# Performance work log

Hardware: AMD Instinct MI355X
Metric: run time of the kernel (lower is better)

Reference implementation:

```python
import jax, jax.numpy as jnp
import numpy as np
from jax.scipy.special import logsumexp

N, T, K, V = 32, 4096, 128, 50000

def setup_inputs() -> dict:
    key = jax.random.key(0)
    ks = jax.random.split(key, 6)
    return {
        "x": jax.random.randint(ks[0], (N, T), 0, V, dtype=jnp.int64),
        "start_w": jax.random.normal(ks[1], (K, 1), dtype=jnp.float32),
        "start_b": jax.random.normal(ks[2], (K,), dtype=jnp.float32),
        "cluster_trans_w": jax.random.uniform(ks[3], (K * K, 1), dtype=jnp.float32, minval=-1.0, maxval=1.0),
        "emb_cluster_w": jax.random.normal(ks[4], (K, K), dtype=jnp.float32),
        "cluster_vocab_w": jax.random.uniform(ks[5], (V, K), dtype=jnp.float32, minval=-1.0, maxval=1.0),
    }

def reference(x, start_w, start_b, cluster_trans_w, emb_cluster_w, cluster_vocab_w):
    # dummy = ones(N,1) => Linear(1,.) collapses to weight[:,0] (+ bias), identical per batch row
    tran = jax.nn.log_softmax(cluster_trans_w[:, 0].reshape(K, K), axis=-1)      # (K,K) log p(k'|k)
    alpha0 = jnp.broadcast_to(start_w[:, 0] + start_b, (N, K))                    # (N,K)
    # Emissions[k,v] = log_softmax_v(emb_cluster.weight[k] @ cluster_vocab.weight.T)
    emis_t = jax.nn.log_softmax(emb_cluster_w @ cluster_vocab_w.T, axis=-1).T     # (V,K)

    def step(alpha, w_t):
        a = logsumexp(alpha[:, :, None] + tran[None, :, :], axis=1)               # (N,K)
        a = a + emis_t[w_t]                                                        # gather emission log-probs
        return a, None

    alpha_T, _ = jax.lax.scan(step, alpha0, x.T)                                  # scan over T timesteps
    return -jnp.mean(logsumexp(alpha_T, axis=1))
```

## Files before the change

kernel.cpp:

```cpp
#include <hip/hip_runtime.h>

typedef unsigned int uint;
typedef unsigned short ushort;
typedef uint4 uint4_a __attribute__((may_alias));
typedef uint ui4v __attribute__((ext_vector_type(4)));
typedef float fx4 __attribute__((ext_vector_type(4)));
typedef short s8v __attribute__((ext_vector_type(8)));

__device__ __forceinline__ uint bfpack(float a, float b) {
  uint ua = __float_as_uint(a), ub = __float_as_uint(b);
  ua += 0x7fffu + ((ua >> 16) & 1u);
  ub += 0x7fffu + ((ub >> 16) & 1u);
  return (ua >> 16) | (ub & 0xffff0000u);
}
__device__ __forceinline__ float bflo(uint d) { return __uint_as_float(d << 16); }
__device__ __forceinline__ float bfhi(uint d) { return __uint_as_float(d & 0xffff0000u); }
__device__ __forceinline__ ushort bfr(float s) {
  return (ushort)((__float_as_uint(s) + 0x8000u) >> 16);
}

#if __has_builtin(__builtin_amdgcn_fdot2_f32_bf16)
#define HAVE_BFDOT 1
typedef __bf16 v2bf __attribute__((ext_vector_type(2)));
__device__ __forceinline__ float dot2bf(uint a, uint b, float c) {
  return __builtin_amdgcn_fdot2_f32_bf16(__builtin_bit_cast(v2bf, a),
                                         __builtin_bit_cast(v2bf, b), c, false);
}
#else
#define HAVE_BFDOT 0
#endif

__global__ __launch_bounds__(128) void k_tran(const float* __restrict__ w,
                                              uint* __restrict__ Tcol) {
  __shared__ float rowLSE[128];
  int tid = threadIdx.x;
  const float4* w4 = (const float4*)(w + tid * 128);
  float se = 0.f;
  #pragma unroll 8
  for (int i = 0; i < 32; ++i) {
    float4 v = w4[i];
    se += __expf(v.x) + __expf(v.y) + __expf(v.z) + __expf(v.w);
  }
  rowLSE[tid] = __logf(se);
  __syncthreads();
  int j = tid & 63;
  int c = 2 * blockIdx.x + (tid >> 6);
  float a = __expf(w[(2 * j) * 128 + c]     - rowLSE[2 * j]);
  float b = __expf(w[(2 * j + 1) * 128 + c] - rowLSE[2 * j + 1]);
  Tcol[c * 64 + j] = bfpack(a, b);
}

__global__ __launch_bounds__(256) void k_logits(const float* __restrict__ emb,
    const float* __restrict__ vocab, uint* __restrict__ qtbl,
    float* __restrict__ S_glob, int V) {
  __shared__ float S_part[128];
  int tid = threadIdx.x;
  int kt = tid & 15, vt = tid >> 4;
  int k0 = kt * 8;
  int vbase = blockIdx.x * 64 + vt * 4;
  if (tid < 128) S_part[tid] = 0.f;
  __syncthreads();

  float acc[4][8];
  #pragma unroll
  for (int i = 0; i < 4; ++i)
    #pragma unroll
    for (int r = 0; r < 8; ++r) acc[i][r] = 0.f;

  int vidx[4];
  #pragma unroll
  for (int i = 0; i < 4; ++i) { int vv = vbase + i; vidx[i] = (vv < V) ? vv : (V - 1); }

  const float4* emb4 = (const float4*)emb;
  const float4* voc4 = (const float4*)vocab;
  for (int jb = 0; jb < 32; ++jb) {
    float4 e4[8];
    #pragma unroll
    for (int r = 0; r < 8; ++r) e4[r] = emb4[(k0 + r) * 32 + jb];
    #pragma unroll
    for (int i = 0; i < 4; ++i) {
      float4 va = voc4[(size_t)vidx[i] * 32 + jb];
      #pragma unroll
      for (int r = 0; r < 8; ++r)
        acc[i][r] += va.x * e4[r].x + va.y * e4[r].y + va.z * e4[r].z + va.w * e4[r].w;
    }
  }

  float sume[8];
  #pragma unroll
  for (int r = 0; r < 8; ++r) sume[r] = 0.f;
  #pragma unroll
  for (int i = 0; i < 4; ++i) {
    int vv = vbase + i;
    if (vv < V) {
      #pragma unroll
      for (int r = 0; r < 8; ++r) sume[r] += __expf(acc[i][r]);
      uint4 st;
      st.x = bfpack(acc[i][0], acc[i][1]);
      st.y = bfpack(acc[i][2], acc[i][3]);
      st.z = bfpack(acc[i][4], acc[i][5]);
      st.w = bfpack(acc[i][6], acc[i][7]);
      *((uint4*)(qtbl + (size_t)vv * 64) + kt) = st;
    }
  }
  #pragma unroll
  for (int r = 0; r < 8; ++r) atomicAdd(&S_part[k0 + r], sume[r]);
  __syncthreads();
  if (tid < 128) atomicAdd(&S_glob[tid], S_part[tid]);
}

__global__ __launch_bounds__(256) void k_qtab(uint* __restrict__ qtbl,
    const float* __restrict__ S_glob, float* __restrict__ Emax, int V) {
  int tid = threadIdx.x;
  int l = tid & 63;
  int v = blockIdx.x * 4 + (tid >> 6);
  if (v >= V) return;
  float2 S2 = ((const float2*)S_glob)[l];
  float z0 = __logf(S2.x), z1 = __logf(S2.y);
  size_t off = (size_t)v * 64 + l;
  uint d = qtbl[off];
  float e0 = bflo(d) - z0, e1 = bfhi(d) - z1;
  float m = fmaxf(e0, e1);
  #pragma unroll
  for (int s = 1; s < 64; s <<= 1) m = fmaxf(m, __shfl_xor(m, s, 64));
  float q0 = __expf(e0 - m), q1 = __expf(e1 - m);
  qtbl[off] = bfpack(q0, q1);
  if (l == 0) Emax[v] = m;
}

#define REPB(M) M(0,0) M(0,1) M(0,2) M(0,3) M(1,0) M(1,1) M(1,2) M(1,3) \
                M(2,0) M(2,1) M(2,2) M(2,3) M(3,0) M(3,1) M(3,2) M(3,3) \
                M(4,0) M(4,1) M(4,2) M(4,3) M(5,0) M(5,1) M(5,2) M(5,3) \
                M(6,0) M(6,1) M(6,2) M(6,3) M(7,0) M(7,1) M(7,2) M(7,3)

#define MFMA(a, b, c) __builtin_amdgcn_mfma_f32_16x16x32_bf16( \
    __builtin_bit_cast(s8v, a), __builtin_bit_cast(s8v, b), c, 0, 0, 0)

#define MST0(OUT, BN) \
  OUT##0 = MFMA(tb0_0, BN, zz4); OUT##1 = MFMA(tb1_0, BN, zz4); \
  OUT##2 = MFMA(tb2_0, BN, zz4); OUT##3 = MFMA(tb3_0, BN, zz4); \
  OUT##4 = MFMA(tb4_0, BN, zz4); OUT##5 = MFMA(tb5_0, BN, zz4); \
  OUT##6 = MFMA(tb6_0, BN, zz4); OUT##7 = MFMA(tb7_0, BN, zz4);
#define MSTA(OUT, BN, ks) \
  OUT##0 = MFMA(tb0_##ks, BN, OUT##0); OUT##1 = MFMA(tb1_##ks, BN, OUT##1); \
  OUT##2 = MFMA(tb2_##ks, BN, OUT##2); OUT##3 = MFMA(tb3_##ks, BN, OUT##3); \
  OUT##4 = MFMA(tb4_##ks, BN, OUT##4); OUT##5 = MFMA(tb5_##ks, BN, OUT##5); \
  OUT##6 = MFMA(tb6_##ks, BN, OUT##6); OUT##7 = MFMA(tb7_##ks, BN, OUT##7);

#define PKPAIR(CCA, CCB, QA, QB, DOUT) { \
  float f0 = bflo(QA.x) * rs, f1 = bfhi(QA.x) * rs; \
  float f2 = bflo(QA.y) * rs, f3 = bfhi(QA.y) * rs; \
  float s0 = CCA.x * f0, s1 = CCA.y * f1, s2 = CCA.z * f2, s3 = CCA.w * f3; \
  fm = fmaxf(fm, fmaxf(fmaxf(s0, s1), fmaxf(s2, s3))); \
  uint p0, p1, p2, p3; \
  asm("v_cvt_pk_bf16_f32 %0, %1, %2" : "=v"(p0) : "v"(s0), "v"(s1)); \
  asm("v_cvt_pk_bf16_f32 %0, %1, %2" : "=v"(p1) : "v"(s2), "v"(s3)); \
  float g0 = bflo(QB.x) * rs, g1 = bfhi(QB.x) * rs; \
  float g2 = bflo(QB.y) * rs, g3 = bfhi(QB.y) * rs; \
  float t0 = CCB.x * g0, t1 = CCB.y * g1, t2 = CCB.z * g2, t3 = CCB.w * g3; \
  fm = fmaxf(fm, fmaxf(fmaxf(t0, t1), fmaxf(t2, t3))); \
  asm("v_cvt_pk_bf16_f32 %0, %1, %2" : "=v"(p2) : "v"(t0), "v"(t1)); \
  asm("v_cvt_pk_bf16_f32 %0, %1, %2" : "=v"(p3) : "v"(t2), "v"(t3)); \
  DOUT.x = p0; DOUT.y = p1; DOUT.z = p2; DOUT.w = p3; }

#define PKPAIR_NR(CCA, CCB, QA, QB, DOUT) { \
  float s0 = CCA.x * bflo(QA.x), s1 = CCA.y * bfhi(QA.x); \
  float s2 = CCA.z * bflo(QA.y), s3 = CCA.w * bfhi(QA.y); \
  uint p0, p1, p2, p3; \
  asm("v_cvt_pk_bf16_f32 %0, %1, %2" : "=v"(p0) : "v"(s0), "v"(s1)); \
  asm("v_cvt_pk_bf16_f32 %0, %1, %2" : "=v"(p1) : "v"(s2), "v"(s3)); \
  float t0 = CCB.x * bflo(QB.x), t1 = CCB.y * bfhi(QB.x); \
  float t2 = CCB.z * bflo(QB.y), t3 = CCB.w * bfhi(QB.y); \
  asm("v_cvt_pk_bf16_f32 %0, %1, %2" : "=v"(p2) : "v"(t0), "v"(t1)); \
  asm("v_cvt_pk_bf16_f32 %0, %1, %2" : "=v"(p3) : "v"(t2), "v"(t3)); \
  DOUT.x = p0; DOUT.y = p1; DOUT.z = p2; DOUT.w = p3; }

#define QLD(dst, tk, i) dst = *(const uint2*)(qtbl + ((size_t)(tk) << 6) + 8 * (i) + 2 * quad);

#define QRELOAD(Q, TKREG, FBASE) \
  QLD(Q##0, TKREG, 0) QLD(Q##1, TKREG, 1) QLD(Q##2, TKREG, 2) QLD(Q##3, TKREG, 3) \
  QLD(Q##4, TKREG, 4) QLD(Q##5, TKREG, 5) QLD(Q##6, TKREG, 6) QLD(Q##7, TKREG, 7) \
  { int fi_ = (FBASE) + 4; if (fi_ > 511) fi_ = 511; TKREG = xseg[fi_]; }

#define SLOT_RS(CIN, COUT, Q, TKREG, FBASE) { \
  rs = 1.0f / fmA;  llacc += __log2f(fmA); \
  float fm = 0.f; \
  PKPAIR(CIN##0, CIN##1, Q##0, Q##1, Bs0) \
  MST0(COUT, Bs0) \
  PKPAIR(CIN##2, CIN##3, Q##2, Q##3, Bs1) \
  MSTA(COUT, Bs1, 1) \
  PKPAIR(CIN##4, CIN##5, Q##4, Q##5, Bs2) \
  MSTA(COUT, Bs2, 2) \
  PKPAIR(CIN##6, CIN##7, Q##6, Q##7, Bs3) \
  MSTA(COUT, Bs3, 3) \
  QRELOAD(Q, TKREG, FBASE) \
  fm = fmaxf(fm, __shfl_xor(fm, 16, 64)); \
  fm = fmaxf(fm, __shfl_xor(fm, 32, 64)); \
  fmA = fmaxf(fm, 1e-33f); \
}

#define SLOT_NR(CIN, COUT, Q, TKREG, FBASE) { \
  PKPAIR_NR(CIN##0, CIN##1, Q##0, Q##1, Bs0) \
  MST0(COUT, Bs0) \
  PKPAIR_NR(CIN##2, CIN##3, Q##2, Q##3, Bs1) \
  MSTA(COUT, Bs1, 1) \
  PKPAIR_NR(CIN##4, CIN##5, Q##4, Q##5, Bs2) \
  MSTA(COUT, Bs2, 2) \
  PKPAIR_NR(CIN##6, CIN##7, Q##6, Q##7, Bs3) \
  MSTA(COUT, Bs3, 3) \
  QRELOAD(Q, TKREG, FBASE) \
}

__global__ __attribute__((amdgpu_flat_work_group_size(512, 512), amdgpu_waves_per_eu(2)))
void k_seg(const int* __restrict__ x, const uint* __restrict__ Tcol,
           const uint* __restrict__ qtbl, uint* __restrict__ Pst,
           float* __restrict__ LLseg) {
  int tid = threadIdx.x;
  int wv = tid >> 6, l = tid & 63, c = l & 15, quad = l >> 4;
  int blk = blockIdx.x;
  const int* xseg = x + (size_t)(blk >> 3) * 4096 + (size_t)(blk & 7) * 512;

  #define DECLB(nt, ks) ui4v tb##nt##_##ks;
  REPB(DECLB)
  {
    #define LOADB(nt, ks) { \
      const uint2* t2_ = (const uint2*)(Tcol + (size_t)(16 * (nt) + c) * 64 + 16 * (ks) + 2 * quad); \
      uint2 lo_ = t2_[0], hi_ = t2_[4]; \
      tb##nt##_##ks.x = lo_.x; tb##nt##_##ks.y = lo_.y; \
      tb##nt##_##ks.z = hi_.x; tb##nt##_##ks.w = hi_.y; }
    REPB(LOADB)
    #define PINB(nt, ks) asm volatile("" : "+a"(tb##nt##_##ks));
    REPB(PINB)
  }

  ui4v Bs0, Bs1, Bs2, Bs3;
  {
    uint iv = (quad == (c >> 2)) ? (0x3F80u << (16 * (c & 1))) : 0u;
    int dsel = ((c >> 1) & 1) + 2 * (wv & 1);
    int kssel = wv >> 1;
    Bs0.x = (kssel == 0 && dsel == 0) ? iv : 0u;
    Bs0.y = (kssel == 0 && dsel == 1) ? iv : 0u;
    Bs0.z = (kssel == 0 && dsel == 2) ? iv : 0u;
    Bs0.w = (kssel == 0 && dsel == 3) ? iv : 0u;
    Bs1.x = (kssel == 1 && dsel == 0) ? iv : 0u;
    Bs1.y = (kssel == 1 && dsel == 1) ? iv : 0u;
    Bs1.z = (kssel == 1 && dsel == 2) ? iv : 0u;
    Bs1.w = (kssel == 1 && dsel == 3) ? iv : 0u;
    Bs2.x = (kssel == 2 && dsel == 0) ? iv : 0u;
    Bs2.y = (kssel == 2 && dsel == 1) ? iv : 0u;
    Bs2.z = (kssel == 2 && dsel == 2) ? iv : 0u;
    Bs2.w = (kssel == 2 && dsel == 3) ? iv : 0u;
    Bs3.x = (kssel == 3 && dsel == 0) ? iv : 0u;
    Bs3.y = (kssel == 3 && dsel == 1) ? iv : 0u;
    Bs3.z = (kssel == 3 && dsel == 2) ? iv : 0u;
    Bs3.w = (kssel == 3 && dsel == 3) ? iv : 0u;
  }

  float rs = 1.0f, llacc = 0.0f, fmA = 1.0f;
  fx4 zz4; zz4.x = 0.f; zz4.y = 0.f; zz4.z = 0.f; zz4.w = 0.f;

  fx4 cA0, cA1, cA2, cA3, cA4, cA5, cA6, cA7;
  fx4 cB0, cB1, cB2, cB3, cB4, cB5, cB6, cB7;

  int tk0 = xseg[0], tk1 = xseg[1];
  int tkA = xseg[2], tkB = xseg[3];
  uint2 qc0, qc1, qc2, qc3, qc4, qc5, qc6, qc7;
  uint2 qn0, qn1, qn2, qn3, qn4, qn5, qn6, qn7;
  QLD(qc0, tk0, 0) QLD(qc1, tk0, 1) QLD(qc2, tk0, 2) QLD(qc3, tk0, 3)
  QLD(qc4, tk0, 4) QLD(qc5, tk0, 5) QLD(qc6, tk0, 6) QLD(qc7, tk0, 7)
  QLD(qn0, tk1, 0) QLD(qn1, tk1, 1) QLD(qn2, tk1, 2) QLD(qn3, tk1, 3)
  QLD(qn4, tk1, 4) QLD(qn5, tk1, 5) QLD(qn6, tk1, 6) QLD(qn7, tk1, 7)

  MST0(cA, Bs0) MSTA(cA, Bs1, 1) MSTA(cA, Bs2, 2) MSTA(cA, Bs3, 3)

  if (wv & 1) __builtin_amdgcn_s_sleep(8);

  for (int f4 = 0; f4 < 128; ++f4) {
    int f = f4 * 4;
    SLOT_RS(cA, cB, qc, tkA, f)
    SLOT_NR(cB, cA, qn, tkB, f + 1)
    SLOT_NR(cA, cB, qc, tkA, f + 2)
    SLOT_NR(cB, cA, qn, tkB, f + 3)
  }

  size_t pb = (size_t)blk * 8192 + (size_t)(16 * wv + c) * 64;
  uint2 st;
  st.x = Bs0.x; st.y = Bs0.y; *(uint2*)(Pst + pb +  0 + 2 * quad) = st;
  st.x = Bs0.z; st.y = Bs0.w; *(uint2*)(Pst + pb +  8 + 2 * quad) = st;
  st.x = Bs1.x; st.y = Bs1.y; *(uint2*)(Pst + pb + 16 + 2 * quad) = st;
  st.x = Bs1.z; st.y = Bs1.w; *(uint2*)(Pst + pb + 24 + 2 * quad) = st;
  st.x = Bs2.x; st.y = Bs2.y; *(uint2*)(Pst + pb + 32 + 2 * quad) = st;
  st.x = Bs2.z; st.y = Bs2.w; *(uint2*)(Pst + pb + 40 + 2 * quad) = st;
  st.x = Bs3.x; st.y = Bs3.y; *(uint2*)(Pst + pb + 48 + 2 * quad) = st;
  st.x = Bs3.z; st.y = Bs3.w; *(uint2*)(Pst + pb + 56 + 2 * quad) = st;
  if (quad == 0)
    LLseg[(size_t)blk * 128 + 16 * wv + c] = llacc * 0.6931471805599453f;
}

__global__ __launch_bounds__(256, 1) void k_comb(
    const float* __restrict__ start_w, const float* __restrict__ start_b,
    const uint* __restrict__ Pst, const float* __restrict__ LLseg,
    float* __restrict__ chainLL) {
  __shared__ uint al[64] __attribute__((aligned(16)));
  __shared__ float2 part[4][64];
  int n = blockIdx.x, tid = threadIdx.x;
  int wv = tid >> 6, l = tid & 63;
  float p0 = 0.f, p1 = 0.f, LLacc = 0.f;
  if (wv == 0) {
    float a0i = start_w[2 * l] + start_b[2 * l];
    float a1i = start_w[2 * l + 1] + start_b[2 * l + 1];
    float m = fmaxf(a0i, a1i);
    #pragma unroll
    for (int s = 1; s < 64; s <<= 1) m = fmaxf(m, __shfl_xor(m, s, 64));
    p0 = __expf(a0i - m); p1 = __expf(a1i - m);
    float tot = p0 + p1;
    #pragma unroll
    for (int s = 1; s < 64; s <<= 1) tot += __shfl_xor(tot, s, 64);
    LLacc = m + __logf(tot);
    float inv = 1.0f / tot;
    p0 *= inv; p1 *= inv;
  }
  const uint4_a* u4 = (const uint4_a*)al;

  for (int s = 0; s < 8; ++s) {
    float g = 0.f;
    if (wv == 0) {
      float La = LLseg[(size_t)(n * 8 + s) * 128 + 2 * l];
      float Lb = LLseg[(size_t)(n * 8 + s) * 128 + 2 * l + 1];
      g = fmaxf(La, Lb);
      #pragma unroll
      for (int sh = 1; sh < 64; sh <<= 1) g = fmaxf(g, __shfl_xor(g, sh, 64));
      al[l] = bfpack(p0 * __expf(La - g), p1 * __expf(Lb - g));
    }
    __syncthreads();

    const uint* pb = Pst + (size_t)(n * 8 + s) * 8192;
    float o0 = 0.f, o1 = 0.f;
    #pragma unroll
    for (int ii = 0; ii < 4; ++ii) {
      int i = 4 * wv + ii;
      uint4 uu = u4[i];
      #pragma unroll
      for (int d = 0; d < 4; ++d) {
        uint ad = (d == 0) ? uu.x : (d == 1) ? uu.y : (d == 2) ? uu.z : uu.w;
        uint P0 = pb[(8 * i + 2 * d) * 64 + l];
        uint P1 = pb[(8 * i + 2 * d + 1) * 64 + l];
        float alo = bflo(ad), ahi = bfhi(ad);
        o0 = fmaf(alo, bflo(P0), o0); o0 = fmaf(ahi, bflo(P1), o0);
        o1 = fmaf(alo, bfhi(P0), o1); o1 = fmaf(ahi, bfhi(P1), o1);
      }
    }
    part[wv][l] = make_float2(o0, o1);
    __syncthreads();

    if (wv == 0) {
      float2 x0 = part[0][l], x1 = part[1][l], x2 = part[2][l], x3 = part[3][l];
      float s0 = (x0.x + x1.x) + (x2.x + x3.x);
      float s1 = (x0.y + x1.y) + (x2.y + x3.y);
      float tt = s0 + s1;
      #pragma unroll
      for (int sh = 1; sh < 64; sh <<= 1) tt += __shfl_xor(tt, sh, 64);
      LLacc += g + __logf(tt);
      float it = 1.0f / tt;
      p0 = s0 * it; p1 = s1 * it;
    }
  }
  if (tid == 0) chainLL[n] = LLacc;
}

#define RLU(i) ((uint)__builtin_amdgcn_readlane((int)ud, rbase + (i)))
#if HAVE_BFDOT
#define DOTS \
  uint u0=RLU(0),u1=RLU(1),u2=RLU(2),u3=RLU(3),u4=RLU(4),u5=RLU(5),u6=RLU(6),u7=RLU(7), \
       u8=RLU(8),u9=RLU(9),u10=RLU(10),u11=RLU(11),u12=RLU(12),u13=RLU(13),u14=RLU(14),u15=RLU(15); \
  float A0 = dot2bf(u0, tA0.x, 0.f), A1 = dot2bf(u1, tA0.y, 0.f); \
  float A2 = dot2bf(u2, tA0.z, 0.f), A3 = dot2bf(u3, tA0.w, 0.f); \
  float B0 = dot2bf(u0, tB0.x, 0.f), B1 = dot2bf(u1, tB0.y, 0.f); \
  float B2 = dot2bf(u2, tB0.z, 0.f), B3 = dot2bf(u3, tB0.w, 0.f); \
  A0 = dot2bf(u4, tA1.x, A0); A1 = dot2bf(u5, tA1.y, A1); \
  A2 = dot2bf(u6, tA1.z, A2); A3 = dot2bf(u7, tA1.w, A3); \
  B0 = dot2bf(u4, tB1.x, B0); B1 = dot2bf(u5, tB1.y, B1); \
  B2 = dot2bf(u6, tB1.z, B2); B3 = dot2bf(u7, tB1.w, B3); \
  A0 = dot2bf(u8, tA2.x, A0); A1 = dot2bf(u9, tA2.y, A1); \
  A2 = dot2bf(u10, tA2.z, A2); A3 = dot2bf(u11, tA2.w, A3); \
  B0 = dot2bf(u8, tB2.x, B0); B1 = dot2bf(u9, tB2.y, B1); \
  B2 = dot2bf(u10, tB2.z, B2); B3 = dot2bf(u11, tB2.w, B3); \
  A0 = dot2bf(u12, tA3.x, A0); A1 = dot2bf(u13, tA3.y, A1); \
  A2 = dot2bf(u14, tA3.z, A2); A3 = dot2bf(u15, tA3.w, A3); \
  B0 = dot2bf(u12, tB3.x, B0); B1 = dot2bf(u13, tB3.y, B1); \
  B2 = dot2bf(u14, tB3.z, B2); B3 = dot2bf(u15, tB3.w, B3); \
  float Asum = (A0 + A1) + (A2 + A3), Bsum = (B0 + B1) + (B2 + B3);
#else
#define ACC2(i, AA, BB) { uint tu = RLU(i); float lo = bflo(tu), hi = bfhi(tu); \
  AA += lo * fa##i.x; AA += hi * fa##i.y; BB += lo * fb##i.x; BB += hi * fb##i.y; }
#define DOTS \
  float A0 = 0.f, A1 = 0.f, A2 = 0.f, A3 = 0.f; \
  float B0 = 0.f, B1 = 0.f, B2 = 0.f, B3 = 0.f; \
  ACC2(0, A0, B0) ACC2(1, A1, B1) ACC2(2, A2, B2) ACC2(3, A3, B3) \
  ACC2(4, A0, B0) ACC2(5, A1, B1) ACC2(6, A2, B2) ACC2(7, A3, B3) \
  ACC2(8, A0, B0) ACC2(9, A1, B1) ACC2(10, A2, B2) ACC2(11, A3, B3) \
  ACC2(12, A0, B0) ACC2(13, A1, B1) ACC2(14, A2, B2) ACC2(15, A3, B3) \
  float Asum = (A0 + A1) + (A2 + A3), Bsum = (B0 + B1) + (B2 + B3);
#endif

#define STEPF(j, p) { \
  DOTS \
  *(float2*)&partLDS[(p) * 640 + l * 10 + 2 * wv] = make_float2(Asum, Bsum); \
  asm volatile("s_waitcnt lgkmcnt(0)\ns_barrier" ::: "memory"); \
  const float2* pr = (const float2*)&partLDS[(p) * 640 + l * 10]; \
  float2 x0 = pr[0], x1 = pr[1], x2 = pr[2], x3 = pr[3]; \
  float s0 = (x0.x + x1.x) + (x2.x + x3.x); \
  float s1 = (x0.y + x1.y) + (x2.y + x3.y); \
  float nu0 = s0 * bflo(qc##j), nu1 = s1 * bfhi(qc##j); \
  qc##j = qtbl[(size_t)tk##j * 64 + l]; \
  tk##j = xrow[(tbase + (j) + 16) & 4095]; \
  if ((j) == 7) { \
    float tt = nu0 + nu1; \
    for (int s = 1; s < 64; s <<= 1) tt += __shfl_xor(tt, s, 64); \
    LLacc += __logf(tt); \
    float it = 1.0f / tt; nu0 *= it; nu1 *= it; \
  } \
  ud = bfpack(nu0, nu1); }

__global__ __launch_bounds__(256, 1) void k_chain(const int* __restrict__ x,
    const float* __restrict__ start_w, const float* __restrict__ start_b,
    const uint* __restrict__ Tcol, const uint* __restrict__ qtbl,
    float* __restrict__ chainLL) {
  __shared__ float partLDS[1280];
  int n = blockIdx.x;
  int l = threadIdx.x & 63;
  int wv = __builtin_amdgcn_readfirstlane((int)(threadIdx.x >> 6));
  int rbase = wv * 16;
  const int* xrow = x + (size_t)n * 4096;

  const uint4* ca = (const uint4*)(Tcol + (2 * l) * 64 + rbase);
  const uint4* cb = (const uint4*)(Tcol + (2 * l + 1) * 64 + rbase);
  uint4 tA0 = ca[0], tA1 = ca[1], tA2 = ca[2], tA3 = ca[3];
  uint4 tB0 = cb[0], tB1 = cb[1], tB2 = cb[2], tB3 = cb[3];
#if !HAVE_BFDOT
  float2 fa0 = make_float2(bflo(tA0.x), bfhi(tA0.x)), fa1 = make_float2(bflo(tA0.y), bfhi(tA0.y));
  float2 fa2 = make_float2(bflo(tA0.z), bfhi(tA0.z)), fa3 = make_float2(bflo(tA0.w), bfhi(tA0.w));
  float2 fa4 = make_float2(bflo(tA1.x), bfhi(tA1.x)), fa5 = make_float2(bflo(tA1.y), bfhi(tA1.y));
  float2 fa6 = make_float2(bflo(tA1.z), bfhi(tA1.z)), fa7 = make_float2(bflo(tA1.w), bfhi(tA1.w));
  float2 fa8 = make_float2(bflo(tA2.x), bfhi(tA2.x)), fa9 = make_float2(bflo(tA2.y), bfhi(tA2.y));
  float2 fa10 = make_float2(bflo(tA2.z), bfhi(tA2.z)), fa11 = make_float2(bflo(tA2.w), bfhi(tA2.w));
  float2 fa12 = make_float2(bflo(tA3.x), bfhi(tA3.x)), fa13 = make_float2(bflo(tA3.y), bfhi(tA3.y));
  float2 fa14 = make_float2(bflo(tA3.z), bfhi(tA3.z)), fa15 = make_float2(bflo(tA3.w), bfhi(tA3.w));
  float2 fb0 = make_float2(bflo(tB0.x), bfhi(tB0.x)), fb1 = make_float2(bflo(tB0.y), bfhi(tB0.y));
  float2 fb2 = make_float2(bflo(tB0.z), bfhi(tB0.z)), fb3 = make_float2(bflo(tB0.w), bfhi(tB0.w));
  float2 fb4 = make_float2(bflo(tB1.x), bfhi(tB1.x)), fb5 = make_float2(bflo(tB1.y), bfhi(tB1.y));
  float2 fb6 = make_float2(bflo(tB1.z), bfhi(tB1.z)), fb7 = make_float2(bflo(tB1.w), bfhi(tB1.w));
  float2 fb8 = make_float2(bflo(tB2.x), bfhi(tB2.x)), fb9 = make_float2(bflo(tB2.y), bfhi(tB2.y));
  float2 fb10 = make_float2(bflo(tB2.z), bfhi(tB2.z)), fb11 = make_float2(bflo(tB2.w), bfhi(tB2.w));
  float2 fb12 = make_float2(bflo(tB3.x), bfhi(tB3.x)), fb13 = make_float2(bflo(tB3.y), bfhi(tB3.y));
  float2 fb14 = make_float2(bflo(tB3.z), bfhi(tB3.z)), fb15 = make_float2(bflo(tB3.w), bfhi(tB3.w));
#endif

  float a0i = start_w[2 * l] + start_b[2 * l];
  float a1i = start_w[2 * l + 1] + start_b[2 * l + 1];
  float m = fmaxf(a0i, a1i);
  #pragma unroll
  for (int s = 1; s < 64; s <<= 1) m = fmaxf(m, __shfl_xor(m, s, 64));
  float p0 = __expf(a0i - m), p1 = __expf(a1i - m);
  float tot = p0 + p1;
  #pragma unroll
  for (int s = 1; s < 64; s <<= 1) tot += __shfl_xor(tot, s, 64);
  float LLacc = m + __logf(tot);
  float inv = 1.0f / tot;
  uint ud = bfpack(p0 * inv, p1 * inv);

  uint qc0 = qtbl[(size_t)xrow[0] * 64 + l], qc1 = qtbl[(size_t)xrow[1] * 64 + l];
  uint qc2 = qtbl[(size_t)xrow[2] * 64 + l], qc3 = qtbl[(size_t)xrow[3] * 64 + l];
  uint qc4 = qtbl[(size_t)xrow[4] * 64 + l], qc5 = qtbl[(size_t)xrow[5] * 64 + l];
  uint qc6 = qtbl[(size_t)xrow[6] * 64 + l], qc7 = qtbl[(size_t)xrow[7] * 64 + l];
  int tk0 = xrow[8],  tk1 = xrow[9],  tk2 = xrow[10], tk3 = xrow[11];
  int tk4 = xrow[12], tk5 = xrow[13], tk6 = xrow[14], tk7 = xrow[15];

  for (int t8 = 0; t8 < 512; ++t8) {
    int tbase = t8 * 8;
    STEPF(0, 0) STEPF(1, 1) STEPF(2, 0) STEPF(3, 1)
    STEPF(4, 0) STEPF(5, 1) STEPF(6, 0) STEPF(7, 1)
  }
  if (l == 0 && wv == 0) chainLL[n] = LLacc;
}

__global__ __launch_bounds__(256) void k_emaxsum(const int* __restrict__ x,
    const float* __restrict__ Emax, float* __restrict__ sumE, int NT) {
  int idx = blockIdx.x * 256 + threadIdx.x;
  float s = 0.f;
  for (; idx < NT; idx += 128 * 256) s += Emax[x[idx]];
  #pragma unroll
  for (int mk = 1; mk < 64; mk <<= 1) s += __shfl_xor(s, mk, 64);
  if ((threadIdx.x & 63) == 0) atomicAdd(sumE, s);
}

__global__ void k_final(const float* __restrict__ chainLL, const float* __restrict__ sumE,
                        float* __restrict__ out, int N) {
  int l = threadIdx.x;
  float v = (l < N) ? chainLL[l] : 0.f;
  #pragma unroll
  for (int mk = 1; mk < 64; mk <<= 1) v += __shfl_xor(v, mk, 64);
  if (l == 0) out[0] = -(v + sumE[0]) / (float)N;
}

extern "C" void kernel_launch(void* const* d_in, const int* in_sizes, int n_in,
                              void* d_out, int out_size, void* d_ws, size_t ws_size,
                              hipStream_t stream) {
  if (n_in < 6) return;
  const int*   x       = (const int*)d_in[0];
  const float* start_w = (const float*)d_in[1];
  const float* start_b = (const float*)d_in[2];
  const float* trans_w = (const float*)d_in[3];
  const float* emb_w   = (const float*)d_in[4];
  const float* vocab_w = (const float*)d_in[5];
  int NT = in_sizes[0];
  int N  = NT / 4096;
  int V  = in_sizes[5] / 128;

  char* ws = (char*)d_ws;
  float* S_glob  = (float*)(ws + 0);
  float* sumE    = (float*)(ws + 512);
  float* chainLL = (float*)(ws + 768);
  uint*  Tcol    = (uint*)(ws + 1024);
  float* Emax    = (float*)(ws + 36864);
  uint*  qtbl    = (uint*)(ws + 262144);
  size_t pst_off = 262144 + (size_t)V * 256;
  uint*  Pst     = (uint*)(ws + pst_off);
  size_t llseg_off = pst_off + (size_t)N * 8 * 8192 * 4;
  float* LLseg   = (float*)(ws + llseg_off);
  size_t need    = llseg_off + (size_t)N * 8 * 128 * 4 + 64;

  hipMemsetAsync(d_ws, 0, 1024, stream);
  k_tran<<<dim3(64), dim3(128), 0, stream>>>(trans_w, Tcol);
  k_logits<<<dim3((V + 63) / 64), dim3(256), 0, stream>>>(emb_w, vocab_w, qtbl, S_glob, V);
  k_qtab<<<dim3((V + 3) / 4), dim3(256), 0, stream>>>(qtbl, S_glob, Emax, V);
  if (ws_size >= need) {
    k_seg<<<dim3(N * 8), dim3(512), 0, stream>>>(x, Tcol, qtbl, Pst, LLseg);
    k_comb<<<dim3(N), dim3(256), 0, stream>>>(start_w, start_b, Pst, LLseg, chainLL);
  } else {
    k_chain<<<dim3(N), dim3(256), 0, stream>>>(x, start_w, start_b, Tcol, qtbl, chainLL);
  }
  k_emaxsum<<<dim3(128), dim3(256), 0, stream>>>(x, Emax, sumE, NT);
  k_final<<<dim3(1), dim3(64), 0, stream>>>(chainLL, sumE, (float*)d_out, N);
}
```

Measured before the change: 698.2 us.

## Compute emission logits with bf16 MFMA instead of scalar FP32 FMAs

Replaces the scalar FP32 emission-logit GEMM (50000x128x128) with bf16 MFMA 16x16x32 instructions. A new small kernel pre-packs the embedding matrix into bf16 pairs, and each wave holds it in AGPRs. Vocab rows are converted to bf16 on the fly with v_cvt_pk_bf16_f32. Logits now carry bf16 input rounding, adding precision error, and an extra kernel launch is added. The workspace layout is also reshuffled to make room for the packed embedding.

```diff
diff --git a/kernel.cpp b/kernel.cpp
--- a/kernel.cpp
+++ b/kernel.cpp
@@ -18,6 +18,9 @@
 __device__ __forceinline__ ushort bfr(float s) {
   return (ushort)((__float_as_uint(s) + 0x8000u) >> 16);
 }
+__device__ __forceinline__ uint cvtpk(float a, float b) {
+  uint r; asm("v_cvt_pk_bf16_f32 %0, %1, %2" : "=v"(r) : "v"(a), "v"(b)); return r;
+}
 
 #if __has_builtin(__builtin_amdgcn_fdot2_f32_bf16)
 #define HAVE_BFDOT 1
@@ -29,6 +32,14 @@
 #else
 #define HAVE_BFDOT 0
 #endif
+
+#define REPB(M) M(0,0) M(0,1) M(0,2) M(0,3) M(1,0) M(1,1) M(1,2) M(1,3) \
+                M(2,0) M(2,1) M(2,2) M(2,3) M(3,0) M(3,1) M(3,2) M(3,3) \
+                M(4,0) M(4,1) M(4,2) M(4,3) M(5,0) M(5,1) M(5,2) M(5,3) \
+                M(6,0) M(6,1) M(6,2) M(6,3) M(7,0) M(7,1) M(7,2) M(7,3)
+
+#define MFMA(a, b, c) __builtin_amdgcn_mfma_f32_16x16x32_bf16( \
+    __builtin_bit_cast(s8v, a), __builtin_bit_cast(s8v, b), c, 0, 0, 0)
 
 __global__ __launch_bounds__(128) void k_tran(const float* __restrict__ w,
                                               uint* __restrict__ Tcol) {
@@ -50,61 +61,79 @@
   Tcol[c * 64 + j] = bfpack(a, b);
 }
 
-__global__ __launch_bounds__(256) void k_logits(const float* __restrict__ emb,
-    const float* __restrict__ vocab, uint* __restrict__ qtbl,
-    float* __restrict__ S_glob, int V) {
+__global__ __launch_bounds__(256) void k_epack(const float* __restrict__ emb,
+                                               uint* __restrict__ Ecol) {
+  int t = blockIdx.x * 256 + threadIdx.x;
+  if (t >= 8192) return;
+  float2 e = *(const float2*)(emb + 2 * t);
+  Ecol[t] = bfpack(e.x, e.y);
+}
+
+__global__ __attribute__((amdgpu_flat_work_group_size(256, 256)))
+void k_logits(const float* __restrict__ vocab, const uint* __restrict__ Ecol,
+              uint* __restrict__ qtbl, float* __restrict__ S_glob, int V) {
   __shared__ float S_part[128];
-  int tid = threadIdx.x;
-  int kt = tid & 15, vt = tid >> 4;
-  int k0 = kt * 8;
-  int vbase = blockIdx.x * 64 + vt * 4;
+  int tid = threadIdx.x, wv = tid >> 6, l = tid & 63, c = l & 15, quad = l >> 4;
   if (tid < 128) S_part[tid] = 0.f;
   __syncthreads();
 
-  float acc[4][8];
-  #pragma unroll
-  for (int i = 0; i < 4; ++i)
-    #pragma unroll
-    for (int r = 0; r < 8; ++r) acc[i][r] = 0.f;
-
-  int vidx[4];
-  #pragma unroll
-  for (int i = 0; i < 4; ++i) { int vv = vbase + i; vidx[i] = (vv < V) ? vv : (V - 1); }
-
-  const float4* emb4 = (const float4*)emb;
-  const float4* voc4 = (const float4*)vocab;
-  for (int jb = 0; jb < 32; ++jb) {
-    float4 e4[8];
-    #pragma unroll
-    for (int r = 0; r < 8; ++r) e4[r] = emb4[(k0 + r) * 32 + jb];
-    #pragma unroll
-    for (int i = 0; i < 4; ++i) {
-      float4 va = voc4[(size_t)vidx[i] * 32 + jb];
-      #pragma unroll
-      for (int r = 0; r < 8; ++r)
-        acc[i][r] += va.x * e4[r].x + va.y * e4[r].y + va.z * e4[r].z + va.w * e4[r].w;
-    }
-  }
-
-  float sume[8];
-  #pragma unroll
-  for (int r = 0; r < 8; ++r) sume[r] = 0.f;
-  #pragma unroll
-  for (int i = 0; i < 4; ++i) {
-    int vv = vbase + i;
-    if (vv < V) {
-      #pragma unroll
-      for (int r = 0; r < 8; ++r) sume[r] += __expf(acc[i][r]);
-      uint4 st;
-      st.x = bfpack(acc[i][0], acc[i][1]);
-      st.y = bfpack(acc[i][2], acc[i][3]);
-      st.z = bfpack(acc[i][4], acc[i][5]);
-      st.w = bfpack(acc[i][6], acc[i][7]);
-      *((uint4*)(qtbl + (size_t)vv * 64) + kt) = st;
-    }
-  }
-  #pragma unroll
-  for (int r = 0; r < 8; ++r) atomicAdd(&S_part[k0 + r], sume[r]);
+  int vb = blockIdx.x * 64 + wv * 16;
+  int vrow = vb + c; if (vrow > V - 1) vrow = V - 1;
+
+  #define DECLE(kt, ks) ui4v eb##kt##_##ks;
+  REPB(DECLE)
+  {
+    #define LOADE(kt, ks) { \
+      const uint2* t2_ = (const uint2*)(Ecol + (size_t)(16 * (kt) + c) * 64 + 16 * (ks) + 2 * quad); \
+      uint2 lo_ = t2_[0], hi_ = t2_[4]; \
+      eb##kt##_##ks.x = lo_.x; eb##kt##_##ks.y = lo_.y; \
+      eb##kt##_##ks.z = hi_.x; eb##kt##_##ks.w = hi_.y; }
+    REPB(LOADE)
+    #define PINE(kt, ks) asm volatile("" : "+a"(eb##kt##_##ks));
+    REPB(PINE)
+  }
+
+  const float4* vr = (const float4*)(vocab + (size_t)vrow * 128);
+  ui4v va0, va1, va2, va3;
+  #define MKVA(ks, dst) { \
+    float4 a_ = vr[8 * (ks) + quad]; \
+    float4 b_ = vr[8 * (ks) + 4 + quad]; \
+    dst.x = cvtpk(a_.x, a_.y); dst.y = cvtpk(a_.z, a_.w); \
+    dst.z = cvtpk(b_.x, b_.y); dst.w = cvtpk(b_.z, b_.w); }
+  MKVA(0, va0) MKVA(1, va1) MKVA(2, va2) MKVA(3, va3)
+
+  fx4 zz4; zz4.x = 0.f; zz4.y = 0.f; zz4.z = 0.f; zz4.w = 0.f;
+  #define CCKT(kt) \
+    fx4 cc##kt = MFMA(va0, eb##kt##_0, zz4); \
+    cc##kt = MFMA(va1, eb##kt##_1, cc##kt); \
+    cc##kt = MFMA(va2, eb##kt##_2, cc##kt); \
+    cc##kt = MFMA(va3, eb##kt##_3, cc##kt);
+  CCKT(0) CCKT(1) CCKT(2) CCKT(3) CCKT(4) CCKT(5) CCKT(6) CCKT(7)
+
+  int v0 = vb + 4 * quad;
+  #define ESUM(kt) { \
+    float se_ = 0.f; \
+    if (v0 + 0 < V) se_ += __expf(cc##kt.x); \
+    if (v0 + 1 < V) se_ += __expf(cc##kt.y); \
+    if (v0 + 2 < V) se_ += __expf(cc##kt.z); \
+    if (v0 + 3 < V) se_ += __expf(cc##kt.w); \
+    atomicAdd(&S_part[16 * (kt) + c], se_); }
+  ESUM(0) ESUM(1) ESUM(2) ESUM(3) ESUM(4) ESUM(5) ESUM(6) ESUM(7)
+
+  #define STKT(kt) { \
+    float nx_ = __shfl_xor(cc##kt.x, 1, 64); \
+    float ny_ = __shfl_xor(cc##kt.y, 1, 64); \
+    float nz_ = __shfl_xor(cc##kt.z, 1, 64); \
+    float nw_ = __shfl_xor(cc##kt.w, 1, 64); \
+    if (!(c & 1)) { \
+      int j_ = 8 * (kt) + (c >> 1); \
+      if (v0 + 0 < V) qtbl[(size_t)(v0 + 0) * 64 + j_] = bfpack(cc##kt.x, nx_); \
+      if (v0 + 1 < V) qtbl[(size_t)(v0 + 1) * 64 + j_] = bfpack(cc##kt.y, ny_); \
+      if (v0 + 2 < V) qtbl[(size_t)(v0 + 2) * 64 + j_] = bfpack(cc##kt.z, nz_); \
+      if (v0 + 3 < V) qtbl[(size_t)(v0 + 3) * 64 + j_] = bfpack(cc##kt.w, nw_); \
+    } }
+  STKT(0) STKT(1) STKT(2) STKT(3) STKT(4) STKT(5) STKT(6) STKT(7)
+
   __syncthreads();
   if (tid < 128) atomicAdd(&S_glob[tid], S_part[tid]);
 }
@@ -127,14 +156,6 @@
   qtbl[off] = bfpack(q0, q1);
   if (l == 0) Emax[v] = m;
 }
-
-#define REPB(M) M(0,0) M(0,1) M(0,2) M(0,3) M(1,0) M(1,1) M(1,2) M(1,3) \
-                M(2,0) M(2,1) M(2,2) M(2,3) M(3,0) M(3,1) M(3,2) M(3,3) \
-                M(4,0) M(4,1) M(4,2) M(4,3) M(5,0) M(5,1) M(5,2) M(5,3) \
-                M(6,0) M(6,1) M(6,2) M(6,3) M(7,0) M(7,1) M(7,2) M(7,3)
-
-#define MFMA(a, b, c) __builtin_amdgcn_mfma_f32_16x16x32_bf16( \
-    __builtin_bit_cast(s8v, a), __builtin_bit_cast(s8v, b), c, 0, 0, 0)
 
 #define MST0(OUT, BN) \
   OUT##0 = MFMA(tb0_0, BN, zz4); OUT##1 = MFMA(tb1_0, BN, zz4); \
@@ -522,9 +543,12 @@
   float* sumE    = (float*)(ws + 512);
   float* chainLL = (float*)(ws + 768);
   uint*  Tcol    = (uint*)(ws + 1024);
-  float* Emax    = (float*)(ws + 36864);
-  uint*  qtbl    = (uint*)(ws + 262144);
-  size_t pst_off = 262144 + (size_t)V * 256;
+  uint*  Ecol    = (uint*)(ws + 36864);
+  float* Emax    = (float*)(ws + 73728);
+  size_t qtbl_off = 73728 + (size_t)V * 4;
+  qtbl_off = (qtbl_off + 255) & ~(size_t)255;
+  uint*  qtbl    = (uint*)(ws + qtbl_off);
+  size_t pst_off = qtbl_off + (size_t)V * 256;
   uint*  Pst     = (uint*)(ws + pst_off);
   size_t llseg_off = pst_off + (size_t)N * 8 * 8192 * 4;
   float* LLseg   = (float*)(ws + llseg_off);
@@ -532,7 +556,8 @@
 
   hipMemsetAsync(d_ws, 0, 1024, stream);
   k_tran<<<dim3(64), dim3(128), 0, stream>>>(trans_w, Tcol);
-  k_logits<<<dim3((V + 63) / 64), dim3(256), 0, stream>>>(emb_w, vocab_w, qtbl, S_glob, V);
+  k_epack<<<dim3(32), dim3(256), 0, stream>>>(emb_w, Ecol);
+  k_logits<<<dim3((V + 63) / 64), dim3(256), 0, stream>>>(vocab_w, Ecol, qtbl, S_glob, V);
   k_qtab<<<dim3((V + 3) / 4), dim3(256), 0, stream>>>(qtbl, S_glob, Emax, V);
   if (ws_size >= need) {
     k_seg<<<dim3(N * 8), dim3(512), 0, stream>>>(x, Tcol, qtbl, Pst, LLseg);
```

After: 616.6 us. -11.7%, faster.
